# Optimization experiments

Measured on AMD Instinct MI355X. Metric: run time of the kernel, lower is better.

Reference implementation:

```python
import jax, jax.numpy as jnp
import numpy as np

OUT, IN, GS = 8192, 8192, 128
N_GROUPS = OUT * IN // GS  # 524288


def setup_inputs() -> dict:
    key = jax.random.key(0)
    k1, k2, k3 = jax.random.split(key, 3)
    x = jax.random.normal(k1, (32, IN), dtype=jnp.float32)
    # ternary values in {-1, 0, 1}
    ternary = jax.random.randint(k2, (OUT, IN), -1, 2, dtype=jnp.int32)
    # positive per-group scales
    scales = jax.random.uniform(k3, (N_GROUPS,), dtype=jnp.float32, minval=0.01, maxval=0.1)
    return {"x": x, "ternary": ternary, "scales": scales}


def reference(x, ternary, scales):
    # Dequantize: each contiguous group of GS weights shares one scale.
    # scales: [n_groups] -> [n_groups, GS] -> [OUT, IN]
    scales_exp = jnp.broadcast_to(scales[:, None], (N_GROUPS, GS)).reshape(OUT, IN)
    w = ternary.astype(jnp.float32) * scales_exp  # [OUT, IN]
    # F.linear(x, w) = x @ w.T
    return jnp.einsum("ti,oi->to", x, w)
```

## Files before the change

kernel.cpp:

```cpp
#include <hip/hip_runtime.h>
#include <stdint.h>

#define OUT_DIM 8192
#define IN_DIM  8192
#define GS      128
#define MROWS   32
#define NSPLIT  8
#define KCHUNK  1024
#define KSTG    128
#define NSTG    (KCHUNK / KSTG)
#define PART_ELEMS (MROWS * OUT_DIM)

typedef __attribute__((ext_vector_type(8))) short bf16x8;
typedef __attribute__((ext_vector_type(4))) float f32x4;
typedef __attribute__((ext_vector_type(8))) unsigned short u16x8;
typedef __attribute__((ext_vector_type(2))) unsigned short u16x2;
typedef __attribute__((ext_vector_type(4))) unsigned int   u32x4;

__device__ __forceinline__ unsigned short f2bf_rne(float f) {
    uint32_t v = __builtin_bit_cast(uint32_t, f);
    v += 0x7FFFu + ((v >> 16) & 1u);
    return (unsigned short)(v >> 16);
}

__global__ __launch_bounds__(256) void prep_xbf(const float* __restrict__ x,
                                                unsigned short* __restrict__ xbf) {
    int i = (blockIdx.x * 256 + threadIdx.x) * 8;
    float4 a = *(const float4*)(x + i);
    float4 b = *(const float4*)(x + i + 4);
    float f[8] = {a.x, a.y, a.z, a.w, b.x, b.y, b.z, b.w};
    u16x8 u;
#pragma unroll
    for (int j = 0; j < 8; ++j) u[j] = f2bf_rne(f[j]);
    *(u16x8*)(xbf + i) = u;
}

__device__ __forceinline__ unsigned int cvt2(int t0, int t1, unsigned int p32) {
    unsigned int t16 = __builtin_amdgcn_perm((unsigned int)t1, (unsigned int)t0,
                                             0x05040100u);
    unsigned int v   = p32 | (t16 & 0x80008000u);
    u16x2 r = __builtin_bit_cast(u16x2, v) *
              __builtin_bit_cast(u16x2, t16 & 0x00010001u);
    return __builtin_bit_cast(unsigned int, r);
}

__device__ __forceinline__ bf16x8 conv8(const int4 wa, const int4 wb, unsigned int p32) {
    u32x4 d;
    d[0] = cvt2(wa.x, wa.y, p32);
    d[1] = cvt2(wa.z, wa.w, p32);
    d[2] = cvt2(wb.x, wb.y, p32);
    d[3] = cvt2(wb.z, wb.w, p32);
    return __builtin_bit_cast(bf16x8, d);
}

__device__ __forceinline__ void glds16(const int* g, int* l) {
    __builtin_amdgcn_global_load_lds(
        (const __attribute__((address_space(1))) void*)g,
        (__attribute__((address_space(3))) void*)l, 16, 0, 0);
}

__global__ __launch_bounds__(256) void ternary_gemm(
    const int* __restrict__ tern, const float* __restrict__ scales,
    const unsigned short* __restrict__ xbf, float* __restrict__ part) {
    __shared__ __align__(16) int lw[2][64][KSTG];

    const int tid  = threadIdx.x;
    const int wv   = tid >> 6;
    const int lane = tid & 63;
    const int n    = lane & 15;
    const int quad = lane >> 4;

    const int otile = blockIdx.x & 127;
    const int kc    = blockIdx.x >> 7;
    const int o0    = otile << 6;
    const int o     = o0 + (wv << 4) + n;
    const int kpos0 = kc << 10;

    const int rbase = (wv << 4);
    const int* __restrict__ gstg =
        tern + kpos0 + ((lane & 31) << 2) + (size_t)(o0 + rbase + (lane >> 5)) * IN_DIM;

    const unsigned short* __restrict__ xr0 = xbf + n * IN_DIM + kpos0 + (quad << 3);
    const unsigned short* __restrict__ xr1 = xbf + (16 + n) * IN_DIM + kpos0 + (quad << 3);
    const float* __restrict__ sp = scales + o * (IN_DIM / GS) + (kc << 3);

    f32x4 acc0 = {0.f, 0.f, 0.f, 0.f};
    f32x4 acc1 = {0.f, 0.f, 0.f, 0.f};

#define GLDS_STAGE(BUF, STG) do {                                              \
        const int* gs = gstg + (STG) * KSTG;                                   \
        _Pragma("unroll")                                                      \
        for (int i = 0; i < 8; ++i)                                            \
            glds16(gs + (size_t)(i << 1) * IN_DIM,                             \
                   &lw[BUF][rbase + (i << 1)][0]);                             \
    } while (0)

    GLDS_STAGE(0, 0);
    __syncthreads();

    const int lrow = (wv << 4) + n;

#pragma unroll 1
    for (int s = 0; s < NSTG; ++s) {
        const int buf = s & 1;
        if (s + 1 < NSTG) GLDS_STAGE(buf ^ 1, s + 1);
        const unsigned int ph  = f2bf_rne(sp[s]);
        const unsigned int p32 = ph | (ph << 16);
        const int ks = s * KSTG;
#pragma unroll
        for (int half = 0; half < 4; ++half) {
            const int koff = (half << 5) + (quad << 3);
            int4 w0 = *(const int4*)&lw[buf][lrow][koff];
            int4 w1 = *(const int4*)&lw[buf][lrow][koff + 4];
            bf16x8 a0 = *(const bf16x8*)(xr0 + ks + (half << 5));
            bf16x8 a1 = *(const bf16x8*)(xr1 + ks + (half << 5));
            bf16x8 bfr = conv8(w0, w1, p32);
            acc0 = __builtin_amdgcn_mfma_f32_16x16x32_bf16(a0, bfr, acc0, 0, 0, 0);
            acc1 = __builtin_amdgcn_mfma_f32_16x16x32_bf16(a1, bfr, acc1, 0, 0, 0);
        }
        __syncthreads();
    }
#undef GLDS_STAGE

    float* __restrict__ prow = part + (size_t)kc * PART_ELEMS;
#pragma unroll
    for (int r = 0; r < 4; ++r) {
        prow[(quad * 4 + r) * OUT_DIM + o]      = acc0[r];
        prow[(quad * 4 + r + 16) * OUT_DIM + o] = acc1[r];
    }
}

__global__ __launch_bounds__(256) void reduce_parts(const float* __restrict__ part,
                                                    float* __restrict__ out) {
    const int i = (blockIdx.x * 256 + threadIdx.x) * 4;
    float4 s = *(const float4*)(part + i);
#pragma unroll
    for (int kc = 1; kc < NSPLIT; ++kc) {
        float4 v = *(const float4*)(part + (size_t)kc * PART_ELEMS + i);
        s.x += v.x; s.y += v.y; s.z += v.z; s.w += v.w;
    }
    *(float4*)(out + i) = s;
}

extern "C" void kernel_launch(void* const* d_in, const int* in_sizes, int n_in,
                              void* d_out, int out_size, void* d_ws, size_t ws_size,
                              hipStream_t stream) {
    const float* x      = (const float*)d_in[0];
    const int*   tern   = (const int*)d_in[1];
    const float* scales = (const float*)d_in[2];
    float* out = (float*)d_out;

    unsigned short* xbf = (unsigned short*)d_ws;
    float* part = (float*)((char*)d_ws + (512 << 10));

    prep_xbf<<<128, 256, 0, stream>>>(x, xbf);
    ternary_gemm<<<128 * NSPLIT, 256, 0, stream>>>(tern, scales, xbf, part);
    reduce_parts<<<256, 256, 0, stream>>>(part, out);
}
```

Measured before the change: 382.4 us.

## Deepen LDS pipeline, stage x in LDS, swizzle weights, and double K-split

Splits K into 16 chunks of 512 and uses a 4-deep ring of 64-wide weight stages in LDS. Fine-grained vmcnt waits replace per-stage __syncthreads, so the direct global-to-LDS weight loads stay in flight while MFMAs run. The block's x slice is staged in LDS once instead of being reloaded from global memory, and weight rows are XOR-swizzled to avoid LDS bank conflicts. Scales are preloaded up front. The cost is double the partial-sum traffic in the reduction and higher LDS use per block. Dropping the block barrier is also risky: each wave waits only on its own vmcnt, and the x staging uses plain stores that complete before the only barrier.

```diff
diff --git a/kernel.cpp b/kernel.cpp
--- a/kernel.cpp
+++ b/kernel.cpp
@@ -5,10 +5,11 @@
 #define IN_DIM  8192
 #define GS      128
 #define MROWS   32
-#define NSPLIT  8
-#define KCHUNK  1024
-#define KSTG    128
+#define NSPLIT  16
+#define KCHUNK  512
+#define KSTG    64
 #define NSTG    (KCHUNK / KSTG)
+#define DEPTH   4
 #define PART_ELEMS (MROWS * OUT_DIM)
 
 typedef __attribute__((ext_vector_type(8))) short bf16x8;
@@ -62,7 +63,8 @@
 __global__ __launch_bounds__(256) void ternary_gemm(
     const int* __restrict__ tern, const float* __restrict__ scales,
     const unsigned short* __restrict__ xbf, float* __restrict__ part) {
-    __shared__ __align__(16) int lw[2][64][KSTG];
+    __shared__ __align__(16) int            lw[DEPTH][64][KSTG];
+    __shared__ __align__(16) unsigned short lx[32][KCHUNK + 8];
 
     const int tid  = threadIdx.x;
     const int wv   = tid >> 6;
@@ -74,53 +76,75 @@
     const int kc    = blockIdx.x >> 7;
     const int o0    = otile << 6;
     const int o     = o0 + (wv << 4) + n;
-    const int kpos0 = kc << 10;
+    const int kpos0 = kc << 9;
 
-    const int rbase = (wv << 4);
-    const int* __restrict__ gstg =
-        tern + kpos0 + ((lane & 31) << 2) + (size_t)(o0 + rbase + (lane >> 5)) * IN_DIM;
+    {
+        const int xrow = tid >> 3;
+        const int xc0  = (tid & 7) << 3;
+        const unsigned short* xs = xbf + (size_t)xrow * IN_DIM + kpos0;
+#pragma unroll
+        for (int j = 0; j < 8; ++j) {
+            const int cs = xc0 + (j << 6);
+            *(bf16x8*)&lx[xrow][cs] = *(const bf16x8*)(xs + cs);
+        }
+    }
 
-    const unsigned short* __restrict__ xr0 = xbf + n * IN_DIM + kpos0 + (quad << 3);
-    const unsigned short* __restrict__ xr1 = xbf + (16 + n) * IN_DIM + kpos0 + (quad << 3);
-    const float* __restrict__ sp = scales + o * (IN_DIM / GS) + (kc << 3);
+    const float* __restrict__ sp = scales + o * (IN_DIM / GS) + (kc << 2);
+    unsigned int pga[4];
+#pragma unroll
+    for (int g = 0; g < 4; ++g) {
+        const unsigned int ph = f2bf_rne(sp[g]);
+        pga[g] = ph | (ph << 16);
+    }
+
+    const int rl   = lane >> 4;
+    const int colA = ((lane & 15) << 2) ^ (rl << 3);
+    const int colB = ((lane & 15) << 2) ^ ((4 + rl) << 3);
+    const int* __restrict__ gw =
+        tern + (size_t)(o0 + (wv << 4) + rl) * IN_DIM + kpos0;
+
+#define GLDS_STAGE(ST) do { const int bu_ = (ST) & 3; const int so_ = (ST) * KSTG; \
+        glds16(gw + so_ + colA,                         &lw[bu_][(wv << 4) +  0][0]); \
+        glds16(gw + (size_t) 4 * IN_DIM + so_ + colB,   &lw[bu_][(wv << 4) +  4][0]); \
+        glds16(gw + (size_t) 8 * IN_DIM + so_ + colA,   &lw[bu_][(wv << 4) +  8][0]); \
+        glds16(gw + (size_t)12 * IN_DIM + so_ + colB,   &lw[bu_][(wv << 4) + 12][0]); \
+    } while (0)
+
+#define VMWAIT(N) do { asm volatile("s_waitcnt vmcnt(" #N ")" ::: "memory");   \
+                       __builtin_amdgcn_sched_barrier(0); } while (0)
 
     f32x4 acc0 = {0.f, 0.f, 0.f, 0.f};
     f32x4 acc1 = {0.f, 0.f, 0.f, 0.f};
 
-#define GLDS_STAGE(BUF, STG) do {                                              \
-        const int* gs = gstg + (STG) * KSTG;                                   \
-        _Pragma("unroll")                                                      \
-        for (int i = 0; i < 8; ++i)                                            \
-            glds16(gs + (size_t)(i << 1) * IN_DIM,                             \
-                   &lw[BUF][rbase + (i << 1)][0]);                             \
-    } while (0)
-
-    GLDS_STAGE(0, 0);
+    GLDS_STAGE(0); GLDS_STAGE(1); GLDS_STAGE(2);
     __syncthreads();
 
-    const int lrow = (wv << 4) + n;
+    const int lrw = (wv << 4) + n;
 
-#pragma unroll 1
+#pragma unroll
     for (int s = 0; s < NSTG; ++s) {
-        const int buf = s & 1;
-        if (s + 1 < NSTG) GLDS_STAGE(buf ^ 1, s + 1);
-        const unsigned int ph  = f2bf_rne(sp[s]);
-        const unsigned int p32 = ph | (ph << 16);
-        const int ks = s * KSTG;
+        if (s < NSTG - 2)      VMWAIT(8);
+        else if (s == NSTG - 2) VMWAIT(4);
+        else                    VMWAIT(0);
+        const unsigned int p32 = pga[s >> 1];
+        const int bu = s & 3;
 #pragma unroll
-        for (int half = 0; half < 4; ++half) {
-            const int koff = (half << 5) + (quad << 3);
-            int4 w0 = *(const int4*)&lw[buf][lrow][koff];
-            int4 w1 = *(const int4*)&lw[buf][lrow][koff + 4];
-            bf16x8 a0 = *(const bf16x8*)(xr0 + ks + (half << 5));
-            bf16x8 a1 = *(const bf16x8*)(xr1 + ks + (half << 5));
+        for (int h = 0; h < 2; ++h) {
+            const int cs  = (h << 5) + (quad << 3);
+            const int csw = cs ^ ((n & 7) << 3);
+            int4 w0 = *(const int4*)&lw[bu][lrw][csw];
+            int4 w1 = *(const int4*)&lw[bu][lrw][csw + 4];
+            const int kl = s * KSTG + cs;
+            bf16x8 a0 = *(const bf16x8*)&lx[n][kl];
+            bf16x8 a1 = *(const bf16x8*)&lx[16 + n][kl];
             bf16x8 bfr = conv8(w0, w1, p32);
             acc0 = __builtin_amdgcn_mfma_f32_16x16x32_bf16(a0, bfr, acc0, 0, 0, 0);
             acc1 = __builtin_amdgcn_mfma_f32_16x16x32_bf16(a1, bfr, acc1, 0, 0, 0);
         }
-        __syncthreads();
+        if (s + 3 < NSTG) GLDS_STAGE(s + 3);
     }
 #undef GLDS_STAGE
+#undef VMWAIT
 
     float* __restrict__ prow = part + (size_t)kc * PART_ELEMS;
 #pragma unroll
@@ -150,8 +174,8 @@
     const float* scales = (const float*)d_in[2];
     float* out = (float*)d_out;
 
-    unsigned short* xbf = (unsigned short*)d_ws;
-    float* part = (float*)((char*)d_ws + (512 << 10));
+    unsigned short* xbf  = (unsigned short*)d_ws;
+    float*          part = (float*)((char*)d_ws + (512 << 10));
 
     prep_xbf<<<128, 256, 0, stream>>>(x, xbf);
     ternary_gemm<<<128 * NSPLIT, 256, 0, stream>>>(tern, scales, xbf, part);
```

New measurement: 401.0 us. 4.9% more time.
